# Kernel optimization log

Measured on AMD Instinct MI355X. Metric: run time of the kernel, lower is better.

The kernel has to match this reference:

```python
import jax, jax.numpy as jnp
import numpy as np

NUM_HEADS = 8
HEAD_DIM = 128
ATTN_SCALE = 0.12


def _rope_tables(T, head_dim, dtype=jnp.float32):
    # half-truncate RoPE from modded-nanogpt: base-freq bounded, half the dims unrotated
    angular_freq = (1.0 / 1024.0) ** jnp.linspace(0.0, 1.0, head_dim // 4, dtype=dtype)
    angular_freq = jnp.concatenate([angular_freq, jnp.zeros(head_dim // 4, dtype=dtype)])  # [D/2]
    t = jnp.arange(T, dtype=dtype)
    theta = t[:, None] * angular_freq[None, :]  # [T, D/2]
    return jnp.cos(theta), jnp.sin(theta)


def _apply_rope(x, cos, sin):
    # x: [B, T, H, D]; cos/sin: [T, D/2]
    x1, x2 = jnp.split(x, 2, axis=-1)
    c = cos[None, :, None, :]
    s = sin[None, :, None, :]
    y1 = x1 * c + x2 * s
    y2 = x2 * c - x1 * s
    return jnp.concatenate([y1, y2], axis=-1)


def _rms_norm(x):
    eps = jnp.asarray(jnp.finfo(x.dtype).eps, x.dtype)
    var = jnp.mean(jnp.square(x), axis=-1, keepdims=True)
    return x * jax.lax.rsqrt(var + eps)


def setup_inputs() -> dict:
    key = jax.random.key(0)
    ks = jax.random.split(key, 4)
    B, T, dim = 1, 4096, 1024
    hdim = NUM_HEADS * HEAD_DIM
    std = 0.5 * dim ** (-0.5)
    bound = (3.0 ** 0.5) * std
    x = jax.random.normal(ks[0], (B, T, dim), dtype=jnp.float32)
    ve = jax.random.normal(ks[1], (B, T, hdim), dtype=jnp.float32)
    qkv_w = jax.random.uniform(ks[2], (3, hdim, dim), dtype=jnp.float32, minval=-bound, maxval=bound)
    lambdas = jnp.array([0.5, 0.5], dtype=jnp.float32)
    c_proj_w = jax.random.normal(ks[3], (dim, hdim), dtype=jnp.float32) * 0.02
    return {"x": x, "ve": ve, "qkv_w": qkv_w, "lambdas": lambdas, "c_proj_w": c_proj_w}


def reference(x, ve, qkv_w, lambdas, c_proj_w):
    B, T, dim = x.shape
    H, D = NUM_HEADS, HEAD_DIM
    # fused QKV projection: qkv_w is [3, H*D, dim]
    w = qkv_w.reshape(3 * H * D, dim)
    qkv = jnp.einsum('btd,fd->btf', x, w).reshape(B, T, 3, H, D)
    q, k, v = qkv[:, :, 0], qkv[:, :, 1], qkv[:, :, 2]  # each [B, T, H, D]
    q = _rms_norm(q)
    k = _rms_norm(k)
    cos, sin = _rope_tables(T, D, dtype=jnp.float32)
    q = _apply_rope(q, cos, sin)
    k = _apply_rope(k, cos, sin)
    # lambda-weighted value blend with value embeddings
    v = lambdas[0] * v + lambdas[1] * ve.reshape(B, T, H, D)
    # causal attention, scale = 0.12
    scores = jnp.einsum('bthd,bshd->bhts', q, k) * ATTN_SCALE  # [B, H, T, T]
    causal = jnp.tril(jnp.ones((T, T), dtype=bool))
    scores = jnp.where(causal[None, None, :, :], scores, jnp.asarray(-jnp.inf, scores.dtype))
    p = jax.nn.softmax(scores, axis=-1)
    y = jnp.einsum('bhts,bshd->bthd', p, v).reshape(B, T, H * D)
    return jnp.einsum('btf,df->btd', y, c_proj_w)
```

## Files before the change

kernel.cpp:

```cpp
#include <hip/hip_runtime.h>
#include <hip/hip_bf16.h>

typedef __attribute__((ext_vector_type(4))) float f32x4;
typedef __attribute__((ext_vector_type(16))) float f32x16;
typedef __attribute__((ext_vector_type(8))) __bf16 bf16x8;
typedef unsigned short u16;
typedef unsigned int u32;
typedef __attribute__((ext_vector_type(4))) u16 u16x4;

__device__ __forceinline__ u16 f2bf(float f) {
    u32 u = __builtin_bit_cast(u32, f);
    u32 r = (u + 0x7FFFu + ((u >> 16) & 1u)) >> 16;
    return (u16)r;
}
__device__ __forceinline__ float bf2f(u16 h) {
    return __builtin_bit_cast(float, ((u32)h) << 16);
}
__device__ __forceinline__ bf16x8 ld_frag(const u16* p) {
    uint4 v = *reinterpret_cast<const uint4*>(p);
    return __builtin_bit_cast(bf16x8, v);
}
__device__ __forceinline__ void gld_lds(const u16* gp, u16* lp) {
    __builtin_amdgcn_global_load_lds(
        (const __attribute__((address_space(1))) u32*)gp,
        (__attribute__((address_space(3))) u32*)lp, 16, 0, 0);
}
__device__ __forceinline__ u32 pk_bf16(float lo, float hi) {
    u32 r;
    asm("v_cvt_pk_bf16_f32 %0, %1, %2" : "=v"(r) : "v"(lo), "v"(hi));
    return r;
}
__device__ __forceinline__ void unp8(uint4 v, float* f) {
    f[0] = bf2f((u16)(v.x & 0xffffu)); f[1] = bf2f((u16)(v.x >> 16));
    f[2] = bf2f((u16)(v.y & 0xffffu)); f[3] = bf2f((u16)(v.y >> 16));
    f[4] = bf2f((u16)(v.z & 0xffffu)); f[5] = bf2f((u16)(v.z >> 16));
    f[6] = bf2f((u16)(v.w & 0xffffu)); f[7] = bf2f((u16)(v.w >> 16));
}

__global__ __launch_bounds__(256) void cvt3(const float* __restrict__ x,
                                            const float* __restrict__ w,
                                            const float* __restrict__ c,
                                            u16* __restrict__ xb,
                                            u16* __restrict__ wb,
                                            u16* __restrict__ cb) {
    int b = blockIdx.x;
    const float* in;
    u16* out;
    int i;
    if (b < 4096)      { in = x; out = xb; i = b * 256 + threadIdx.x; }
    else if (b < 7168) { in = w; out = wb; i = (b - 4096) * 256 + threadIdx.x; }
    else               { in = c; out = cb; i = (b - 7168) * 256 + threadIdx.x; }
    float4 v = reinterpret_cast<const float4*>(in)[i];
    u16x4 o;
    o.x = f2bf(v.x); o.y = f2bf(v.y); o.z = f2bf(v.z); o.w = f2bf(v.w);
    *reinterpret_cast<u16x4*>(out + 4 * (size_t)i) = o;
}

__global__ __launch_bounds__(256) void rope_tab(float* __restrict__ ctab,
                                                float* __restrict__ stab) {
    int i = blockIdx.x * 256 + threadIdx.x;
    int t = i >> 6, j = i & 63;
    float c = 1.0f, s = 0.0f;
    if (j < 32) {
        float f = exp2f(-10.0f * (float)j / 31.0f);
        float th = (float)t * f;
        c = cosf(th); s = sinf(th);
    }
    ctab[i] = c; stab[i] = s;
}

template <bool OUT_BF16>
__global__ __launch_bounds__(256) void gemm_nt(const u16* __restrict__ A,
                                               const u16* __restrict__ B,
                                               void* __restrict__ Cout,
                                               int M, int N, int K, int ldc) {
    __shared__ u16 sA[2][128 * 32];
    __shared__ u16 sB[2][128 * 32];
    const int tid = threadIdx.x;
    const int w = tid >> 6, l = tid & 63;
    const int mb = M >> 7;
    const int bm = blockIdx.x % mb, bn = blockIdx.x / mb;
    const int g = l >> 4, c16 = l & 15;
    const int srow = l >> 2, ssl = l & 3;
    const int wr = w >> 1, wc = w & 1;

    f32x4 acc[4][4] = {};

    auto stage = [&](int bi, int kt) {
#pragma unroll
        for (int cc = 0; cc < 2; ++cc) {
            int c = 2 * w + cc;
            int r = 16 * c + srow;
            int gs = ssl ^ ((r >> 1) & 3);
            gld_lds(A + (size_t)(bm * 128 + r) * K + kt * 32 + gs * 8, &sA[bi][c * 512]);
            gld_lds(B + (size_t)(bn * 128 + r) * K + kt * 32 + gs * 8, &sB[bi][c * 512]);
        }
    };

    const int NT = K >> 5;
    stage(0, 0);
    __syncthreads();
    for (int kt = 0; kt < NT; ++kt) {
        int cur = kt & 1;
        if (kt + 1 < NT) stage(cur ^ 1, kt + 1);
        bf16x8 af[4], bf[4];
#pragma unroll
        for (int mi = 0; mi < 4; ++mi) {
            int r = wr * 64 + mi * 16 + c16;
            int sl = g ^ ((r >> 1) & 3);
            af[mi] = ld_frag(&sA[cur][r * 32 + sl * 8]);
        }
#pragma unroll
        for (int ni = 0; ni < 4; ++ni) {
            int r = wc * 64 + ni * 16 + c16;
            int sl = g ^ ((r >> 1) & 3);
            bf[ni] = ld_frag(&sB[cur][r * 32 + sl * 8]);
        }
#pragma unroll
        for (int mi = 0; mi < 4; ++mi)
#pragma unroll
            for (int ni = 0; ni < 4; ++ni)
                acc[mi][ni] = __builtin_amdgcn_mfma_f32_16x16x32_bf16(
                    af[mi], bf[ni], acc[mi][ni], 0, 0, 0);
        __syncthreads();
    }
#pragma unroll
    for (int mi = 0; mi < 4; ++mi) {
#pragma unroll
        for (int ni = 0; ni < 4; ++ni) {
            int col = bn * 128 + wc * 64 + ni * 16 + c16;
            int row0 = bm * 128 + wr * 64 + mi * 16 + g * 4;
#pragma unroll
            for (int r = 0; r < 4; ++r) {
                if (OUT_BF16)
                    ((u16*)Cout)[(size_t)(row0 + r) * ldc + col] = f2bf(acc[mi][ni][r]);
                else
                    ((float*)Cout)[(size_t)(row0 + r) * ldc + col] = acc[mi][ni][r];
            }
        }
    }
}

__global__ __launch_bounds__(256) void prep(const u16* __restrict__ qkvb,
                                            const float* __restrict__ ve,
                                            const float* __restrict__ lambdas,
                                            const float* __restrict__ ctab,
                                            const float* __restrict__ stab,
                                            u16* __restrict__ Qb, u16* __restrict__ Kb,
                                            u16* __restrict__ Vt) {
    __shared__ u16 sV[128 * 72];
    const int h = blockIdx.x >> 6, tb = blockIdx.x & 63;
    const int tid = threadIdx.x;
    const int trow = tid >> 2, p = tid & 3;
    const int t = tb * 64 + trow;
    const float l0 = lambdas[0], l1 = lambdas[1];
    const int cperm = (trow & 51) | ((trow & 4) << 1) | ((trow & 8) >> 1);

#pragma unroll
    for (int which = 0; which < 2; ++which) {
        const u16* src = qkvb + (size_t)t * 3072 + which * 1024 + h * 128;
        int j0 = p * 16;
        float x1[16], x2[16];
        unp8(*(const uint4*)(src + j0), x1);
        unp8(*(const uint4*)(src + j0 + 8), x1 + 8);
        unp8(*(const uint4*)(src + 64 + j0), x2);
        unp8(*(const uint4*)(src + 64 + j0 + 8), x2 + 8);
        float ss = 0.0f;
#pragma unroll
        for (int e = 0; e < 16; ++e) ss += x1[e] * x1[e] + x2[e] * x2[e];
        ss += __shfl_xor(ss, 1);
        ss += __shfl_xor(ss, 2);
        float rs = rsqrtf(ss * (1.0f / 128.0f) + 1.1920929e-07f);
        float scl = which ? 1.0f : 0.12f;
        rs *= scl;
        u16* dst = (which ? Kb : Qb) + ((size_t)h * 4096 + t) * 128;
#pragma unroll
        for (int e = 0; e < 16; ++e) {
            int j = j0 + e;
            float c = ctab[t * 64 + j], s = stab[t * 64 + j];
            float a = x1[e] * rs, b = x2[e] * rs;
            dst[j] = f2bf(a * c + b * s);
            dst[j + 64] = f2bf(b * c - a * s);
        }
    }
    {
        const u16* vsrc = qkvb + (size_t)t * 3072 + 2048 + h * 128 + p * 32;
        const float* vesrc = ve + (size_t)t * 1024 + h * 128 + p * 32;
#pragma unroll
        for (int q8 = 0; q8 < 4; ++q8) {
            float vf[8];
            unp8(*(const uint4*)(vsrc + q8 * 8), vf);
            float4 e0 = *(const float4*)(vesrc + q8 * 8);
            float4 e1 = *(const float4*)(vesrc + q8 * 8 + 4);
            float ee[8] = {e0.x, e0.y, e0.z, e0.w, e1.x, e1.y, e1.z, e1.w};
#pragma unroll
            for (int j = 0; j < 8; ++j) {
                float vv = l0 * vf[j] + l1 * ee[j];
                sV[(p * 32 + q8 * 8 + j) * 72 + cperm] = f2bf(vv);
            }
        }
    }
    __syncthreads();
    {
        int d = tid >> 1, seg = tid & 1;
        const u16* lsrc = &sV[d * 72 + seg * 32];
        u16* gdst = Vt + ((size_t)h * 128 + d) * 4096 + tb * 64 + seg * 32;
#pragma unroll
        for (int q2 = 0; q2 < 4; ++q2)
            *(uint4*)(gdst + q2 * 8) = *(const uint4*)(lsrc + q2 * 8);
    }
}

__global__ __launch_bounds__(256) void attn(const u16* __restrict__ Qb,
                                            const u16* __restrict__ Kb,
                                            const u16* __restrict__ Vt,
                                            u16* __restrict__ Y) {
    __shared__ u16 smem[3 * 8192];
    const int bid = blockIdx.x;
    const int h = bid & 7;
    const int pid = bid >> 3;
    const int qb = (pid < 32) ? (63 - pid) : (pid - 32);
    const int tid = threadIdx.x;
    const int w = tid >> 6, l = tid & 63;
    const int qh = w & 1, kvh = w >> 1;
    const int l31 = l & 31, hi = l >> 5;
    const int qg = qb * 64 + qh * 32 + l31;
    const int krow = kvh * 32 + l31;

    bf16x8 qf[8];
    {
        const u16* qp = Qb + ((size_t)h * 4096 + qg) * 128;
#pragma unroll
        for (int dk = 0; dk < 8; ++dk) qf[dk] = ld_frag(qp + dk * 16 + hi * 8);
    }

    const u16* kp[4];
    const u16* vp[4];
#pragma unroll
    for (int cc = 0; cc < 4; ++cc) {
        int c = 4 * w + cc;
        int rK = 4 * c + (l >> 4);
        int gsK = (l & 15) ^ (rK & 7);
        kp[cc] = Kb + ((size_t)h * 4096 + rK) * 128 + gsK * 8;
        int rV = 8 * c + (l >> 3);
        int gsV = (l & 7) ^ (rV & 7);
        vp[cc] = Vt + ((size_t)h * 128 + rV) * 4096 + gsV * 8;
    }

    f32x16 o[4] = {};
    float ssum = 0.0f;

#pragma unroll
    for (int cc = 0; cc < 4; ++cc) {
        gld_lds(kp[cc], smem + (4 * w + cc) * 512);
        kp[cc] += 8192;
    }
    __syncthreads();

    const int nt = qb + 1;
    int cur = 0;
    for (int t = 0; t < nt; ++t) {
        if (t + 1 < nt) {
#pragma unroll
            for (int cc = 0; cc < 4; ++cc) {
                gld_lds(kp[cc], smem + (cur ^ 1) * 8192 + (4 * w + cc) * 512);
                kp[cc] += 8192;
            }
        }
#pragma unroll
        for (int cc = 0; cc < 4; ++cc) {
            gld_lds(vp[cc], smem + 16384 + (4 * w + cc) * 512);
            vp[cc] += 64;
        }

        const u16* sKc = smem + cur * 8192;
        f32x16 st = {};
        __builtin_amdgcn_s_setprio(1);
#pragma unroll
        for (int dk = 0; dk < 8; ++dk) {
            int sl = (2 * dk + hi) ^ (krow & 7);
            bf16x8 kf = ld_frag(sKc + krow * 128 + sl * 8);
            st = __builtin_amdgcn_mfma_f32_32x32x16_bf16(kf, qf[dk], st, 0, 0, 0);
        }
        __builtin_amdgcn_s_setprio(0);

        float pv[16];
        if (t == qb) {
#pragma unroll
            for (int r = 0; r < 16; ++r) {
                int kvg = t * 64 + kvh * 32 + (r & 3) + 8 * (r >> 2) + 4 * hi;
                pv[r] = (kvg <= qg) ? __expf(st[r]) : 0.0f;
            }
        } else {
#pragma unroll
            for (int r = 0; r < 16; ++r) pv[r] = __expf(st[r]);
        }
        float ps = 0.0f;
#pragma unroll
        for (int i = 0; i < 16; ++i) ps += pv[i];
        ssum += ps;

        bf16x8 pb[2];
#pragma unroll
        for (int m = 0; m < 2; ++m) {
            uint4 u;
            u.x = pk_bf16(pv[8 * m + 0], pv[8 * m + 1]);
            u.y = pk_bf16(pv[8 * m + 2], pv[8 * m + 3]);
            u.z = pk_bf16(pv[8 * m + 4], pv[8 * m + 5]);
            u.w = pk_bf16(pv[8 * m + 6], pv[8 * m + 7]);
            pb[m] = __builtin_bit_cast(bf16x8, u);
        }

        __syncthreads();

        const u16* sVc = smem + 16384;
        __builtin_amdgcn_s_setprio(1);
#pragma unroll
        for (int m = 0; m < 2; ++m) {
#pragma unroll
            for (int dt = 0; dt < 4; ++dt) {
                int drow = dt * 32 + l31;
                int sl = (4 * kvh + 2 * m + hi) ^ (drow & 7);
                bf16x8 vf = ld_frag(sVc + drow * 64 + sl * 8);
                o[dt] = __builtin_amdgcn_mfma_f32_32x32x16_bf16(vf, pb[m], o[dt], 0, 0, 0);
            }
        }
        __builtin_amdgcn_s_setprio(0);
        __syncthreads();
        cur ^= 1;
    }

    ssum += __shfl_xor(ssum, 32);

    float* sO = (float*)smem;
    float* sS = (float*)smem + 8448;
    if (kvh == 1) {
        float* base = sO + (qh * 32 + l31) * 132;
#pragma unroll
        for (int dt = 0; dt < 4; ++dt)
#pragma unroll
            for (int i = 0; i < 4; ++i) {
                int d0 = dt * 32 + i * 8 + hi * 4;
                float4 v = {o[dt][4 * i + 0], o[dt][4 * i + 1],
                            o[dt][4 * i + 2], o[dt][4 * i + 3]};
                *(float4*)(base + d0) = v;
            }
        if (hi == 0) sS[qh * 32 + l31] = ssum;
    }
    __syncthreads();
    if (kvh == 0) {
        float stot = ssum + sS[qh * 32 + l31];
        float inv = 1.0f / stot;
        const float* base = sO + (qh * 32 + l31) * 132;
        u16* yrow = Y + (size_t)qg * 1024 + h * 128;
#pragma unroll
        for (int dt = 0; dt < 4; ++dt)
#pragma unroll
            for (int i = 0; i < 4; ++i) {
                int d0 = dt * 32 + i * 8 + hi * 4;
                float4 prev = *(const float4*)(base + d0);
                u16x4 ov;
                ov.x = f2bf((o[dt][4 * i + 0] + prev.x) * inv);
                ov.y = f2bf((o[dt][4 * i + 1] + prev.y) * inv);
                ov.z = f2bf((o[dt][4 * i + 2] + prev.z) * inv);
                ov.w = f2bf((o[dt][4 * i + 3] + prev.w) * inv);
                *(u16x4*)(yrow + d0) = ov;
            }
    }
}

extern "C" void kernel_launch(void* const* d_in, const int* in_sizes, int n_in,
                              void* d_out, int out_size, void* d_ws, size_t ws_size,
                              hipStream_t stream) {
    const float* x = (const float*)d_in[0];
    const float* ve = (const float*)d_in[1];
    const float* qkv_w = (const float*)d_in[2];
    const float* lambdas = (const float*)d_in[3];
    const float* c_proj_w = (const float*)d_in[4];

    char* ws = (char*)d_ws;
    size_t o = 0;
    u16* qkvb = (u16*)(ws + o); o += (size_t)4096 * 3072 * 2;
    u16* xb   = (u16*)(ws + o); o += (size_t)4096 * 1024 * 2;
    u16* wb   = (u16*)(ws + o); o += (size_t)3072 * 1024 * 2;
    u16* cb   = (u16*)(ws + o); o += (size_t)1024 * 1024 * 2;
    u16* Qb   = (u16*)(ws + o); o += (size_t)8 * 4096 * 128 * 2;
    u16* Kb   = (u16*)(ws + o); o += (size_t)8 * 4096 * 128 * 2;
    u16* Vt   = (u16*)(ws + o); o += (size_t)8 * 4096 * 128 * 2;
    u16* Yb   = (u16*)(ws + o); o += (size_t)4096 * 1024 * 2;
    float* ctab = (float*)(ws + o); o += (size_t)4096 * 64 * 4;
    float* stab = (float*)(ws + o); o += (size_t)4096 * 64 * 4;

    cvt3<<<8192, 256, 0, stream>>>(x, qkv_w, c_proj_w, xb, wb, cb);
    rope_tab<<<1024, 256, 0, stream>>>(ctab, stab);
    gemm_nt<true><<<32 * 24, 256, 0, stream>>>(xb, wb, qkvb, 4096, 3072, 1024, 3072);
    prep<<<512, 256, 0, stream>>>(qkvb, ve, lambdas, ctab, stab, Qb, Kb, Vt);
    attn<<<512, 256, 0, stream>>>(Qb, Kb, Vt, Yb);
    gemm_nt<false><<<32 * 8, 256, 0, stream>>>(Yb, cb, d_out, 4096, 1024, 1024, 1024);
}
```

Before: 165.9 us.

## Split attention KV range across two blocks and combine partial outputs

```diff
diff --git a/kernel.cpp b/kernel.cpp
--- a/kernel.cpp
+++ b/kernel.cpp
@@ -211,162 +211,192 @@
     }
 }
 
+#define OPHALF 4194304
 __global__ __launch_bounds__(256) void attn(const u16* __restrict__ Qb,
                                             const u16* __restrict__ Kb,
                                             const u16* __restrict__ Vt,
-                                            u16* __restrict__ Y) {
+                                            float* __restrict__ Op,
+                                            float* __restrict__ ssumP) {
     __shared__ u16 smem[3 * 8192];
     const int bid = blockIdx.x;
     const int h = bid & 7;
     const int pid = bid >> 3;
-    const int qb = (pid < 32) ? (63 - pid) : (pid - 32);
+    const int j = pid >> 1;
+    const int half = pid & 1;
     const int tid = threadIdx.x;
     const int w = tid >> 6, l = tid & 63;
     const int qh = w & 1, kvh = w >> 1;
     const int l31 = l & 31, hi = l >> 5;
-    const int qg = qb * 64 + qh * 32 + l31;
     const int krow = kvh * 32 + l31;
 
-    bf16x8 qf[8];
-    {
-        const u16* qp = Qb + ((size_t)h * 4096 + qg) * 128;
-#pragma unroll
-        for (int dk = 0; dk < 8; ++dk) qf[dk] = ld_frag(qp + dk * 16 + hi * 8);
-    }
-
-    const u16* kp[4];
-    const u16* vp[4];
-#pragma unroll
-    for (int cc = 0; cc < 4; ++cc) {
-        int c = 4 * w + cc;
-        int rK = 4 * c + (l >> 4);
-        int gsK = (l & 15) ^ (rK & 7);
-        kp[cc] = Kb + ((size_t)h * 4096 + rK) * 128 + gsK * 8;
-        int rV = 8 * c + (l >> 3);
-        int gsV = (l & 7) ^ (rV & 7);
-        vp[cc] = Vt + ((size_t)h * 128 + rV) * 4096 + gsV * 8;
-    }
-
-    f32x16 o[4] = {};
-    float ssum = 0.0f;
-
-#pragma unroll
-    for (int cc = 0; cc < 4; ++cc) {
-        gld_lds(kp[cc], smem + (4 * w + cc) * 512);
-        kp[cc] += 8192;
-    }
-    __syncthreads();
-
-    const int nt = qb + 1;
-    int cur = 0;
-    for (int t = 0; t < nt; ++t) {
-        if (t + 1 < nt) {
+    for (int seg = 0; seg < 2; ++seg) {
+        const int qb = seg ? (63 - j) : j;
+        const int part = seg ? (1 - half) : half;
+        const int s = (qb + 1) >> 1;
+        const int t0 = part ? s : 0;
+        const int t1 = part ? (qb + 1) : s;
+        const int qg = qb * 64 + qh * 32 + l31;
+
+        bf16x8 qf[8];
+        {
+            const u16* qp = Qb + ((size_t)h * 4096 + qg) * 128;
+#pragma unroll
+            for (int dk = 0; dk < 8; ++dk) qf[dk] = ld_frag(qp + dk * 16 + hi * 8);
+        }
+
+        const u16* kp[4];
+        const u16* vp[4];
+#pragma unroll
+        for (int cc = 0; cc < 4; ++cc) {
+            int c = 4 * w + cc;
+            int rK = 4 * c + (l >> 4);
+            int gsK = (l & 15) ^ (rK & 7);
+            kp[cc] = Kb + ((size_t)h * 4096 + t0 * 64 + rK) * 128 + gsK * 8;
+            int rV = 8 * c + (l >> 3);
+            int gsV = (l & 7) ^ (rV & 7);
+            vp[cc] = Vt + ((size_t)h * 128 + rV) * 4096 + t0 * 64 + gsV * 8;
+        }
+
+        f32x16 o[4] = {};
+        float ssum = 0.0f;
+
+        if (t0 < t1) {
 #pragma unroll
             for (int cc = 0; cc < 4; ++cc) {
-                gld_lds(kp[cc], smem + (cur ^ 1) * 8192 + (4 * w + cc) * 512);
+                gld_lds(kp[cc], smem + (4 * w + cc) * 512);
                 kp[cc] += 8192;
             }
-        }
-#pragma unroll
-        for (int cc = 0; cc < 4; ++cc) {
-            gld_lds(vp[cc], smem + 16384 + (4 * w + cc) * 512);
-            vp[cc] += 64;
-        }
-
-        const u16* sKc = smem + cur * 8192;
-        f32x16 st = {};
-        __builtin_amdgcn_s_setprio(1);
-#pragma unroll
-        for (int dk = 0; dk < 8; ++dk) {
-            int sl = (2 * dk + hi) ^ (krow & 7);
-            bf16x8 kf = ld_frag(sKc + krow * 128 + sl * 8);
-            st = __builtin_amdgcn_mfma_f32_32x32x16_bf16(kf, qf[dk], st, 0, 0, 0);
-        }
-        __builtin_amdgcn_s_setprio(0);
-
-        float pv[16];
-        if (t == qb) {
-#pragma unroll
-            for (int r = 0; r < 16; ++r) {
-                int kvg = t * 64 + kvh * 32 + (r & 3) + 8 * (r >> 2) + 4 * hi;
-                pv[r] = (kvg <= qg) ? __expf(st[r]) : 0.0f;
+            __syncthreads();
+
+            int cur = 0;
+            for (int t = t0; t < t1; ++t) {
+                if (t + 1 < t1) {
+#pragma unroll
+                    for (int cc = 0; cc < 4; ++cc) {
+                        gld_lds(kp[cc], smem + (cur ^ 1) * 8192 + (4 * w + cc) * 512);
+                        kp[cc] += 8192;
+                    }
+                }
+#pragma unroll
+                for (int cc = 0; cc < 4; ++cc) {
+                    gld_lds(vp[cc], smem + 16384 + (4 * w + cc) * 512);
+                    vp[cc] += 64;
+                }
+
+                const u16* sKc = smem + cur * 8192;
+                f32x16 st = {};
+                __builtin_amdgcn_s_setprio(1);
+#pragma unroll
+                for (int dk = 0; dk < 8; ++dk) {
+                    int sl = (2 * dk + hi) ^ (krow & 7);
+                    bf16x8 kf = ld_frag(sKc + krow * 128 + sl * 8);
+                    st = __builtin_amdgcn_mfma_f32_32x32x16_bf16(kf, qf[dk], st, 0, 0, 0);
+                }
+                __builtin_amdgcn_s_setprio(0);
+
+                float pv[16];
+                if (t == qb) {
+#pragma unroll
+                    for (int r = 0; r < 16; ++r) {
+                        int kvg = t * 64 + kvh * 32 + (r & 3) + 8 * (r >> 2) + 4 * hi;
+                        pv[r] = (kvg <= qg) ? __expf(st[r]) : 0.0f;
+                    }
+                } else {
+#pragma unroll
+                    for (int r = 0; r < 16; ++r) pv[r] = __expf(st[r]);
+                }
+                float ps = 0.0f;
+#pragma unroll
+                for (int i = 0; i < 16; ++i) ps += pv[i];
+                ssum += ps;
+
+                bf16x8 pb[2];
+#pragma unroll
+                for (int m = 0; m < 2; ++m) {
+                    uint4 u;
+                    u.x = pk_bf16(pv[8 * m + 0], pv[8 * m + 1]);
+                    u.y = pk_bf16(pv[8 * m + 2], pv[8 * m + 3]);
+                    u.z = pk_bf16(pv[8 * m + 4], pv[8 * m + 5]);
+                    u.w = pk_bf16(pv[8 * m + 6], pv[8 * m + 7]);
+                    pb[m] = __builtin_bit_cast(bf16x8, u);
+                }
+
+                __syncthreads();
+
+                const u16* sVc = smem + 16384;
+                __builtin_amdgcn_s_setprio(1);
+#pragma unroll
+                for (int m = 0; m < 2; ++m) {
+#pragma unroll
+                    for (int dt = 0; dt < 4; ++dt) {
+                        int drow = dt * 32 + l31;
+                        int sl = (4 * kvh + 2 * m + hi) ^ (drow & 7);
+                        bf16x8 vf = ld_frag(sVc + drow * 64 + sl * 8);
+                        o[dt] = __builtin_amdgcn_mfma_f32_32x32x16_bf16(vf, pb[m], o[dt], 0, 0, 0);
+                    }
+                }
+                __builtin_amdgcn_s_setprio(0);
+                __syncthreads();
+                cur ^= 1;
             }
         } else {
-#pragma unroll
-            for (int r = 0; r < 16; ++r) pv[r] = __expf(st[r]);
-        }
-        float ps = 0.0f;
-#pragma unroll
-        for (int i = 0; i < 16; ++i) ps += pv[i];
-        ssum += ps;
-
-        bf16x8 pb[2];
-#pragma unroll
-        for (int m = 0; m < 2; ++m) {
-            uint4 u;
-            u.x = pk_bf16(pv[8 * m + 0], pv[8 * m + 1]);
-            u.y = pk_bf16(pv[8 * m + 2], pv[8 * m + 3]);
-            u.z = pk_bf16(pv[8 * m + 4], pv[8 * m + 5]);
-            u.w = pk_bf16(pv[8 * m + 6], pv[8 * m + 7]);
-            pb[m] = __builtin_bit_cast(bf16x8, u);
-        }
-
+            __syncthreads();
+        }
+
+        ssum += __shfl_xor(ssum, 32);
+
+        float* sO = (float*)smem;
+        float* sS = (float*)smem + 8448;
+        if (kvh == 1) {
+            float* base = sO + (qh * 32 + l31) * 132;
+#pragma unroll
+            for (int dt = 0; dt < 4; ++dt)
+#pragma unroll
+                for (int i = 0; i < 4; ++i) {
+                    int d0 = dt * 32 + i * 8 + hi * 4;
+                    float4 v = {o[dt][4 * i + 0], o[dt][4 * i + 1],
+                                o[dt][4 * i + 2], o[dt][4 * i + 3]};
+                    *(float4*)(base + d0) = v;
+                }
+            if (hi == 0) sS[qh * 32 + l31] = ssum;
+        }
         __syncthreads();
-
-        const u16* sVc = smem + 16384;
-        __builtin_amdgcn_s_setprio(1);
-#pragma unroll
-        for (int m = 0; m < 2; ++m) {
-#pragma unroll
-            for (int dt = 0; dt < 4; ++dt) {
-                int drow = dt * 32 + l31;
-                int sl = (4 * kvh + 2 * m + hi) ^ (drow & 7);
-                bf16x8 vf = ld_frag(sVc + drow * 64 + sl * 8);
-                o[dt] = __builtin_amdgcn_mfma_f32_32x32x16_bf16(vf, pb[m], o[dt], 0, 0, 0);
-            }
-        }
-        __builtin_amdgcn_s_setprio(0);
+        if (kvh == 0) {
+            float stot = ssum + sS[qh * 32 + l31];
+            const float* base = sO + (qh * 32 + l31) * 132;
+            float* orow = Op + (size_t)part * OPHALF + ((size_t)(h * 4096 + qg)) * 128;
+#pragma unroll
+            for (int dt = 0; dt < 4; ++dt)
+#pragma unroll
+                for (int i = 0; i < 4; ++i) {
+                    int d0 = dt * 32 + i * 8 + hi * 4;
+                    float4 prev = *(const float4*)(base + d0);
+                    float4 ov = {o[dt][4 * i + 0] + prev.x, o[dt][4 * i + 1] + prev.y,
+                                 o[dt][4 * i + 2] + prev.z, o[dt][4 * i + 3] + prev.w};
+                    *(float4*)(orow + d0) = ov;
+                }
+            if (hi == 0) ssumP[part * 32768 + h * 4096 + qg] = stot;
+        }
         __syncthreads();
-        cur ^= 1;
-    }
-
-    ssum += __shfl_xor(ssum, 32);
-
-    float* sO = (float*)smem;
-    float* sS = (float*)smem + 8448;
-    if (kvh == 1) {
-        float* base = sO + (qh * 32 + l31) * 132;
-#pragma unroll
-        for (int dt = 0; dt < 4; ++dt)
-#pragma unroll
-            for (int i = 0; i < 4; ++i) {
-                int d0 = dt * 32 + i * 8 + hi * 4;
-                float4 v = {o[dt][4 * i + 0], o[dt][4 * i + 1],
-                            o[dt][4 * i + 2], o[dt][4 * i + 3]};
-                *(float4*)(base + d0) = v;
-            }
-        if (hi == 0) sS[qh * 32 + l31] = ssum;
-    }
-    __syncthreads();
-    if (kvh == 0) {
-        float stot = ssum + sS[qh * 32 + l31];
-        float inv = 1.0f / stot;
-        const float* base = sO + (qh * 32 + l31) * 132;
-        u16* yrow = Y + (size_t)qg * 1024 + h * 128;
-#pragma unroll
-        for (int dt = 0; dt < 4; ++dt)
-#pragma unroll
-            for (int i = 0; i < 4; ++i) {
-                int d0 = dt * 32 + i * 8 + hi * 4;
-                float4 prev = *(const float4*)(base + d0);
-                u16x4 ov;
-                ov.x = f2bf((o[dt][4 * i + 0] + prev.x) * inv);
-                ov.y = f2bf((o[dt][4 * i + 1] + prev.y) * inv);
-                ov.z = f2bf((o[dt][4 * i + 2] + prev.z) * inv);
-                ov.w = f2bf((o[dt][4 * i + 3] + prev.w) * inv);
-                *(u16x4*)(yrow + d0) = ov;
-            }
-    }
+    }
+}
+
+__global__ __launch_bounds__(256) void combine(const float* __restrict__ Op,
+                                               const float* __restrict__ ssumP,
+                                               u16* __restrict__ Y) {
+    int i = blockIdx.x * 256 + threadIdx.x;
+    int d4 = i & 31;
+    int hq = i >> 5;
+    int h = hq >> 12, q = hq & 4095;
+    float4 a = ((const float4*)Op)[i];
+    float4 b = ((const float4*)(Op + OPHALF))[i];
+    float inv = 1.0f / (ssumP[hq] + ssumP[32768 + hq]);
+    u16x4 ov;
+    ov.x = f2bf((a.x + b.x) * inv);
+    ov.y = f2bf((a.y + b.y) * inv);
+    ov.z = f2bf((a.z + b.z) * inv);
+    ov.w = f2bf((a.w + b.w) * inv);
+    *(u16x4*)(Y + (size_t)q * 1024 + h * 128 + d4 * 4) = ov;
 }
 
 extern "C" void kernel_launch(void* const* d_in, const int* in_sizes, int n_in,
@@ -390,11 +420,14 @@
     u16* Yb   = (u16*)(ws + o); o += (size_t)4096 * 1024 * 2;
     float* ctab = (float*)(ws + o); o += (size_t)4096 * 64 * 4;
     float* stab = (float*)(ws + o); o += (size_t)4096 * 64 * 4;
+    float* Op    = (float*)qkvb;
+    float* ssumP = (float*)wb;
 
     cvt3<<<8192, 256, 0, stream>>>(x, qkv_w, c_proj_w, xb, wb, cb);
     rope_tab<<<1024, 256, 0, stream>>>(ctab, stab);
     gemm_nt<true><<<32 * 24, 256, 0, stream>>>(xb, wb, qkvb, 4096, 3072, 1024, 3072);
     prep<<<512, 256, 0, stream>>>(qkvb, ve, lambdas, ctab, stab, Qb, Kb, Vt);
-    attn<<<512, 256, 0, stream>>>(Qb, Kb, Vt, Yb);
+    attn<<<512, 256, 0, stream>>>(Qb, Kb, Vt, Op, ssumP);
+    combine<<<4096, 256, 0, stream>>>(Op, ssumP, Yb);
     gemm_nt<false><<<32 * 8, 256, 0, stream>>>(Yb, cb, d_out, 4096, 1024, 1024, 1024);
 }
```

Result: faster. 147.3 us (-11.2%).
